# Performance work log

Measured on AMD Instinct MI355X. Metric: run time of the kernel, lower is better.

## Reference

```python
import jax, jax.numpy as jnp
import numpy as np

HEAD_DIM = 64
FEAT_H, FEAT_W = 64, 64
ROPE_THETA = 10000.0


def axial_rope_cache(dim, height, width, theta):
    # Matches compute_axial_rope_cache: interleaved cos/sin of shape [H*W, dim]
    theta_dim = (dim // 2) // 2
    freqs = 1.0 / theta ** (jnp.arange(theta_dim, dtype=jnp.float32) * 2.0 / theta_dim)
    t_x = jnp.tile(jnp.arange(width, dtype=jnp.float32)[None, :], (height, 1)).reshape(-1)
    t_y = jnp.tile(jnp.arange(height, dtype=jnp.float32)[:, None], (1, width)).reshape(-1)
    theta_all = jnp.concatenate([jnp.outer(t_x, freqs), jnp.outer(t_y, freqs)], axis=-1)
    cos = jnp.repeat(jnp.cos(theta_all), 2, axis=-1)  # [H*W, dim]
    sin = jnp.repeat(jnp.sin(theta_all), 2, axis=-1)
    return cos, sin


def apply_rope(x, cos, sin):
    # x: [B, H, N, D]; cos/sin: [N, D]
    x1 = x[..., 0::2]
    x2 = x[..., 1::2]
    rot = jnp.stack([-x2, x1], axis=-1).reshape(x.shape)
    return x * cos[None, None] + rot * sin[None, None]


def setup_inputs() -> dict:
    key = jax.random.key(0)
    ks = jax.random.split(key, 11)
    B, Nq, Nk, E, KVD, ID = 1, 4096, 8192, 256, 64, 256
    s_e = 1.0 / np.sqrt(E)
    s_kv = 1.0 / np.sqrt(KVD)
    s_i = 1.0 / np.sqrt(ID)
    return {
        "query": jax.random.normal(ks[0], (B, Nq, E), jnp.float32),
        "key": jax.random.normal(ks[1], (B, Nk, KVD), jnp.float32),
        "value": jax.random.normal(ks[2], (B, Nk, KVD), jnp.float32),
        "Wq": jax.random.normal(ks[3], (E, ID), jnp.float32) * s_e,
        "bq": jnp.zeros((ID,), jnp.float32),
        "Wk": jax.random.normal(ks[4], (KVD, ID), jnp.float32) * s_kv,
        "bk": jnp.zeros((ID,), jnp.float32),
        "Wv": jax.random.normal(ks[5], (KVD, ID), jnp.float32) * s_kv,
        "bv": jnp.zeros((ID,), jnp.float32),
        "Wo": jax.random.normal(ks[6], (ID, E), jnp.float32) * s_i,
        "bo": jnp.zeros((E,), jnp.float32),
        "num_k_exclude_rope": 0,
    }


def reference(query, key, value, Wq, bq, Wk, bk, Wv, bv, Wo, bo, num_k_exclude_rope):
    B, Nq, _ = query.shape
    Nk = key.shape[1]
    H, D = 4, HEAD_DIM

    def split_heads(x):
        b, n, c = x.shape
        return x.reshape(b, n, H, c // H).transpose(0, 2, 1, 3)

    q = split_heads(query @ Wq + bq)  # [B,H,Nq,D]
    k = split_heads(key @ Wk + bk)    # [B,H,Nk,D]
    v = split_heads(value @ Wv + bv)

    cos, sin = axial_rope_cache(D, FEAT_H, FEAT_W, ROPE_THETA)  # [4096, D]
    q = apply_rope(q, cos, sin)

    num_k_rope = Nk - num_k_exclude_rope
    k_spatial = k[:, :, :num_k_rope, :]
    k_other = k[:, :, num_k_rope:, :]
    repeats = num_k_rope // cos.shape[0]  # rope_k_repeat=True
    cos_k = jnp.tile(cos, (repeats, 1))
    sin_k = jnp.tile(sin, (repeats, 1))
    k_spatial = apply_rope(k_spatial, cos_k, sin_k)
    k = jnp.concatenate([k_spatial, k_other], axis=2)

    q = q / jnp.sqrt(jnp.asarray(D, q.dtype))
    scores = jnp.einsum("bhqd,bhkd->bhqk", q, k)
    attn = jax.nn.softmax(scores, axis=-1)
    out = jnp.einsum("bhqk,bhkd->bhqd", attn, v)
    out = out.transpose(0, 2, 1, 3).reshape(B, Nq, H * D)
    return out @ Wo + bo
```

## Files before the change

kernel.cpp:

```cpp
#include <hip/hip_runtime.h>
#include <hip/hip_bf16.h>

#define NQ 4096
#define NK 8192
#define NSPLIT 8
#define KSPAN (NK / NSPLIT)
#define BK 64

#define QSCALE 0.1803368801111204f

typedef short v8s __attribute__((ext_vector_type(8)));
typedef float v4f __attribute__((ext_vector_type(4)));

static __device__ __forceinline__ unsigned short f2bf(float f) {
    unsigned int u = __float_as_uint(f);
    u = (u + 0x7FFFu + ((u >> 16) & 1u)) >> 16;
    return (unsigned short)u;
}
static __device__ __forceinline__ float bf2f(unsigned short h) {
    return __uint_as_float(((unsigned int)h) << 16);
}
static __device__ __forceinline__ unsigned int pkbf(float a, float b) {
    union { __hip_bfloat162 h; unsigned int u; } cv;
    cv.h = __float22bfloat162_rn(make_float2(a, b));
    return cv.u;
}
static __device__ __forceinline__ void split8(const float* a, v8s& hi, v8s& lo) {
#pragma unroll
    for (int j = 0; j < 8; ++j) {
        unsigned short h = f2bf(a[j]);
        hi[j] = (short)h;
        lo[j] = (short)f2bf(a[j] - bf2f(h));
    }
}
static __device__ __forceinline__ void wgather(const float* __restrict__ W,
                                               int k0, int col, v8s& wh, v8s& wl) {
    float wv[8];
#pragma unroll
    for (int j = 0; j < 8; ++j) wv[j] = W[(size_t)(k0 + j) * 256 + col];
    split8(wv, wh, wl);
}
static __device__ __forceinline__ void dma16(const unsigned short* g, unsigned short* l) {
    __builtin_amdgcn_global_load_lds(
        (const __attribute__((address_space(1))) unsigned int*)(const void*)g,
        (__attribute__((address_space(3))) unsigned int*)(void*)l, 16, 0, 0);
}

__global__ __launch_bounds__(256) void qkv_kernel(
    const float* __restrict__ query, const float* __restrict__ key,
    const float* __restrict__ value,
    const float* __restrict__ Wq, const float* __restrict__ Wk,
    const float* __restrict__ Wv,
    const float* __restrict__ bq, const float* __restrict__ bk,
    const float* __restrict__ bv,
    unsigned short* __restrict__ Qb, unsigned short* __restrict__ Kb,
    unsigned short* __restrict__ Vt, const int* __restrict__ nexp)
{
    const int b = blockIdx.x;
    const int t = threadIdx.x, w = t >> 6, lane = t & 63;
    const int quad = lane >> 4, l16 = lane & 15;
    const int colbase = w * 64;

    if (b < 256) {
        const int n0 = b * 16;
        v4f acc[4];
#pragma unroll
        for (int ct = 0; ct < 4; ++ct) {
            const float bb = bq[colbase + ct * 16 + l16];
            acc[ct] = v4f{bb, bb, bb, bb};
        }
        const float* arow = query + (size_t)(n0 + l16) * 256 + quad * 8;
#pragma unroll
        for (int k0 = 0; k0 < 256; k0 += 32) {
            float av[8];
            *(float4*)av = *(const float4*)(arow + k0);
            *(float4*)(av + 4) = *(const float4*)(arow + k0 + 4);
            v8s ah, al;
            split8(av, ah, al);
#pragma unroll
            for (int ct = 0; ct < 4; ++ct) {
                v8s wh, wl;
                wgather(Wq, k0 + quad * 8, colbase + ct * 16 + l16, wh, wl);
                acc[ct] = __builtin_amdgcn_mfma_f32_16x16x32_bf16(al, wh, acc[ct], 0, 0, 0);
                acc[ct] = __builtin_amdgcn_mfma_f32_16x16x32_bf16(ah, wl, acc[ct], 0, 0, 0);
                acc[ct] = __builtin_amdgcn_mfma_f32_16x16x32_bf16(ah, wh, acc[ct], 0, 0, 0);
            }
        }
#pragma unroll
        for (int ct = 0; ct < 4; ++ct) {
            const int d = ct * 16 + l16;
            const int j = d >> 1;
            const float freq = exp2f(-(float)(j & 15) * 1.66096404744368f);
            const bool isx = (j < 16), odd = (d & 1);
#pragma unroll
            for (int r = 0; r < 4; ++r) {
                const int p = n0 + quad * 4 + r;
                const float tpos = isx ? (float)(p & 63) : (float)(p >> 6);
                float sn, cs;
                __sincosf(tpos * freq, &sn, &cs);
                const float x = acc[ct][r];
                const float xp = __shfl_xor(x, 1, 64);
                const float y = odd ? fmaf(x, cs, xp * sn) : fmaf(x, cs, -xp * sn);
                Qb[((size_t)(w * NQ + p) << 6) + d] = f2bf(y * QSCALE);
            }
        }
    } else {
        const bool isK = (b < 768);
        const int n0 = (isK ? (b - 256) : (b - 768)) * 16;
        const float* X = isK ? key : value;
        const float* W = isK ? Wk : Wv;
        const float* bias = isK ? bk : bv;
        v4f acc[4];
#pragma unroll
        for (int ct = 0; ct < 4; ++ct) {
            const float bb = bias[colbase + ct * 16 + l16];
            acc[ct] = v4f{bb, bb, bb, bb};
        }
        const float* arow = X + (size_t)(n0 + l16) * 64 + quad * 8;
#pragma unroll
        for (int k0 = 0; k0 < 64; k0 += 32) {
            float av[8];
            *(float4*)av = *(const float4*)(arow + k0);
            *(float4*)(av + 4) = *(const float4*)(arow + k0 + 4);
            v8s ah, al;
            split8(av, ah, al);
#pragma unroll
            for (int ct = 0; ct < 4; ++ct) {
                v8s wh, wl;
                wgather(W, k0 + quad * 8, colbase + ct * 16 + l16, wh, wl);
                acc[ct] = __builtin_amdgcn_mfma_f32_16x16x32_bf16(al, wh, acc[ct], 0, 0, 0);
                acc[ct] = __builtin_amdgcn_mfma_f32_16x16x32_bf16(ah, wl, acc[ct], 0, 0, 0);
                acc[ct] = __builtin_amdgcn_mfma_f32_16x16x32_bf16(ah, wh, acc[ct], 0, 0, 0);
            }
        }
        if (isK) {
            const int nro = NK - *nexp;
#pragma unroll
            for (int ct = 0; ct < 4; ++ct) {
                const int d = ct * 16 + l16;
                const int j = d >> 1;
                const float freq = exp2f(-(float)(j & 15) * 1.66096404744368f);
                const bool isx = (j < 16), odd = (d & 1);
#pragma unroll
                for (int r = 0; r < 4; ++r) {
                    const int p = n0 + quad * 4 + r;
                    const int pc = p & 4095;
                    const float tpos = isx ? (float)(pc & 63) : (float)(pc >> 6);
                    float sn, cs;
                    __sincosf(tpos * freq, &sn, &cs);
                    const float x = acc[ct][r];
                    const float xp = __shfl_xor(x, 1, 64);
                    float y = odd ? fmaf(x, cs, xp * sn) : fmaf(x, cs, -xp * sn);
                    y = (p < nro) ? y : x;
                    Kb[((size_t)(w * NK + p) << 6) + d] = f2bf(y);
                }
            }
        } else {
#pragma unroll
            for (int ct = 0; ct < 4; ++ct) {
                const int col = colbase + ct * 16 + l16;
                uint2 u = make_uint2(pkbf(acc[ct][0], acc[ct][1]),
                                     pkbf(acc[ct][2], acc[ct][3]));
                *(uint2*)(Vt + (size_t)col * NK + n0 + quad * 4) = u;
            }
        }
    }
}

__global__ __launch_bounds__(256) void attn_kernel(
    const unsigned short* __restrict__ Qb, const unsigned short* __restrict__ Kb,
    const unsigned short* __restrict__ Vt, unsigned short* __restrict__ Opart,
    float* __restrict__ Lbuf)
{
    __shared__ alignas(16) unsigned short Kl[64 * 64];
    __shared__ alignas(16) unsigned short Vl[64 * 64];

    const int blk = blockIdx.x;
    const int s = blk & 7, h = (blk >> 3) & 3, qt = blk >> 5;
    const int t = threadIdx.x;
    const int w = t >> 6, lane = t & 63;
    const int quad = lane >> 4, l16 = lane & 15;

    const int q0 = qt * 128 + w * 32;
    v8s qf[2][2];
#pragma unroll
    for (int g = 0; g < 2; ++g) {
        const unsigned short* qr = Qb + ((size_t)(h * NQ + q0 + g * 16 + l16) << 6) + quad * 8;
        qf[g][0] = *(const v8s*)qr;
        qf[g][1] = *(const v8s*)(qr + 32);
    }

    v4f O[4][2];
#pragma unroll
    for (int dt = 0; dt < 4; ++dt)
#pragma unroll
        for (int g = 0; g < 2; ++g) O[dt][g] = v4f{0.f, 0.f, 0.f, 0.f};
    float psum[2] = {0.f, 0.f};

    const unsigned short* Kbase = Kb + (((size_t)h * NK + s * KSPAN) << 6);
    const unsigned short* Vbase = Vt + (size_t)(h * 64) * NK + s * KSPAN;

    const int srow = lane >> 3;
    const int schunk = (lane & 7) ^ srow;
    const int c0off = ((quad ^ (l16 & 7)) * 8);
    const int c1off = c0off ^ 32;
    int voff[2][2];
#pragma unroll
    for (int tv = 0; tv < 2; ++tv)
#pragma unroll
        for (int h2 = 0; h2 < 2; ++h2)
            voff[tv][h2] = (((4 * tv + 2 * h2 + (quad >> 1)) ^ (l16 & 7)) << 3) + 4 * (quad & 1);

    for (int k0 = 0; k0 < KSPAN; k0 += BK) {
        __syncthreads();
#pragma unroll
        for (int half = 0; half < 2; ++half) {
            const int r0 = w * 16 + half * 8;
            dma16(Kbase + ((size_t)(k0 + r0 + srow) << 6) + schunk * 8, &Kl[r0 * 64]);
            dma16(Vbase + (size_t)(r0 + srow) * NK + k0 + schunk * 8, &Vl[r0 * 64]);
        }
        __syncthreads();

        v8s pf[2][2];
#pragma unroll
        for (int tt = 0; tt < 4; ++tt) {
            const unsigned short* kr = &Kl[(tt * 16 + l16) * 64];
            const v8s kf0 = *(const v8s*)(kr + c0off);
            const v8s kf1 = *(const v8s*)(kr + c1off);
#pragma unroll
            for (int g = 0; g < 2; ++g) {
                v4f a = v4f{0.f, 0.f, 0.f, 0.f};
                a = __builtin_amdgcn_mfma_f32_16x16x32_bf16(kf0, qf[g][0], a, 0, 0, 0);
                a = __builtin_amdgcn_mfma_f32_16x16x32_bf16(kf1, qf[g][1], a, 0, 0, 0);
                const float e0 = __builtin_amdgcn_exp2f(a[0]);
                const float e1 = __builtin_amdgcn_exp2f(a[1]);
                const float e2 = __builtin_amdgcn_exp2f(a[2]);
                const float e3 = __builtin_amdgcn_exp2f(a[3]);
                psum[g] += (e0 + e1) + (e2 + e3);
                unsigned int* pp = (unsigned int*)&pf[g][tt >> 1];
                pp[(tt & 1) * 2 + 0] = pkbf(e0, e1);
                pp[(tt & 1) * 2 + 1] = pkbf(e2, e3);
            }
        }

#pragma unroll
        for (int dt = 0; dt < 4; ++dt) {
            const unsigned short* vr = &Vl[(dt * 16 + l16) * 64];
#pragma unroll
            for (int tv = 0; tv < 2; ++tv) {
                union { v8s s; uint2 u[2]; } vv;
                vv.u[0] = *(const uint2*)(vr + voff[tv][0]);
                vv.u[1] = *(const uint2*)(vr + voff[tv][1]);
#pragma unroll
                for (int g = 0; g < 2; ++g)
                    O[dt][g] = __builtin_amdgcn_mfma_f32_16x16x32_bf16(vv.s, pf[g][tv], O[dt][g], 0, 0, 0);
            }
        }
    }

#pragma unroll
    for (int g = 0; g < 2; ++g) {
        float p = psum[g];
        p += __shfl_xor(p, 16, 64);
        p += __shfl_xor(p, 32, 64);
        psum[g] = p;
    }
    unsigned short* Ob = Opart + (size_t)blk * 8192;
#pragma unroll
    for (int g = 0; g < 2; ++g) {
        const int row = w * 32 + g * 16 + l16;
#pragma unroll
        for (int dt = 0; dt < 4; ++dt) {
            uint2 u = make_uint2(pkbf(O[dt][g][0], O[dt][g][1]),
                                 pkbf(O[dt][g][2], O[dt][g][3]));
            *(uint2*)(Ob + row * 64 + dt * 16 + quad * 4) = u;
        }
        if (quad == 0) Lbuf[blk * 128 + row] = psum[g];
    }
}

__global__ __launch_bounds__(256) void oproj_kernel(
    const unsigned short* __restrict__ Opart, const float* __restrict__ Lbuf,
    const float* __restrict__ Wo, const float* __restrict__ bo,
    float* __restrict__ out)
{
    const int t = threadIdx.x, w = t >> 6, lane = t & 63;
    const int quad = lane >> 4, l16 = lane & 15;
    const int n0 = blockIdx.x * 16, colbase = w * 64;
    const int qt32 = (n0 >> 7) * 32;
    const int rbase = n0 & 127;

    float linv[4];
#pragma unroll
    for (int hh = 0; hh < 4; ++hh) {
        float ls = 0.f;
#pragma unroll
        for (int sp = 0; sp < NSPLIT; ++sp)
            ls += Lbuf[(qt32 + hh * 8 + sp) * 128 + rbase + l16];
        linv[hh] = 1.f / ls;
    }
    v4f acc[4];
#pragma unroll
    for (int ct = 0; ct < 4; ++ct) {
        const float bb = bo[colbase + ct * 16 + l16];
        acc[ct] = v4f{bb, bb, bb, bb};
    }
#pragma unroll
    for (int k0 = 0; k0 < 256; k0 += 32) {
        const int hh = k0 >> 6;
        const int d0 = (k0 & 63) + quad * 8;
        float av[8] = {0.f, 0.f, 0.f, 0.f, 0.f, 0.f, 0.f, 0.f};
#pragma unroll
        for (int sp = 0; sp < NSPLIT; ++sp) {
            const v8s A = *(const v8s*)(Opart + (size_t)(qt32 + hh * 8 + sp) * 8192
                                        + (rbase + l16) * 64 + d0);
#pragma unroll
            for (int j = 0; j < 8; ++j) av[j] += bf2f((unsigned short)A[j]);
        }
#pragma unroll
        for (int j = 0; j < 8; ++j) av[j] *= linv[hh];
        v8s ah, al;
        split8(av, ah, al);
#pragma unroll
        for (int ct = 0; ct < 4; ++ct) {
            v8s wh, wl;
            wgather(Wo, k0 + quad * 8, colbase + ct * 16 + l16, wh, wl);
            acc[ct] = __builtin_amdgcn_mfma_f32_16x16x32_bf16(al, wh, acc[ct], 0, 0, 0);
            acc[ct] = __builtin_amdgcn_mfma_f32_16x16x32_bf16(ah, wl, acc[ct], 0, 0, 0);
            acc[ct] = __builtin_amdgcn_mfma_f32_16x16x32_bf16(ah, wh, acc[ct], 0, 0, 0);
        }
    }
#pragma unroll
    for (int ct = 0; ct < 4; ++ct)
#pragma unroll
        for (int r = 0; r < 4; ++r)
            out[(size_t)(n0 + quad * 4 + r) * 256 + colbase + ct * 16 + l16] = acc[ct][r];
}

extern "C" void kernel_launch(void* const* d_in, const int* in_sizes, int n_in,
                              void* d_out, int out_size, void* d_ws, size_t ws_size,
                              hipStream_t stream) {
    const float* query = (const float*)d_in[0];
    const float* key   = (const float*)d_in[1];
    const float* value = (const float*)d_in[2];
    const float* Wq    = (const float*)d_in[3];
    const float* bq    = (const float*)d_in[4];
    const float* Wk    = (const float*)d_in[5];
    const float* bk    = (const float*)d_in[6];
    const float* Wv    = (const float*)d_in[7];
    const float* bv    = (const float*)d_in[8];
    const float* Wo    = (const float*)d_in[9];
    const float* bo    = (const float*)d_in[10];
    const int*   nex   = (const int*)d_in[11];

    char* ws = (char*)d_ws;
    unsigned short* Qb    = (unsigned short*)(ws);
    unsigned short* Kb    = (unsigned short*)(ws + (size_t)2 * 1024 * 1024);
    unsigned short* Vt    = (unsigned short*)(ws + (size_t)6 * 1024 * 1024);
    unsigned short* Opart = (unsigned short*)(ws + (size_t)10 * 1024 * 1024);
    float* Lbuf           = (float*)(ws + (size_t)26 * 1024 * 1024);
    float* out            = (float*)d_out;

    qkv_kernel<<<1280, 256, 0, stream>>>(query, key, value, Wq, Wk, Wv,
                                         bq, bk, bv, Qb, Kb, Vt, nex);
    attn_kernel<<<1024, 256, 0, stream>>>(Qb, Kb, Vt, Opart, Lbuf);
    oproj_kernel<<<256, 256, 0, stream>>>(Opart, Lbuf, Wo, bo, out);
}
```

Before: 168.4 us.

## Pre-split weights into bf16 hi/lo fragment layout and split O reduction from projection

Adds a prep kernel that converts every weight matrix once per call into packed bf16 hi/lo fragments laid out for the MFMA operand, so the GEMM kernels do one vector load instead of eight strided scalar loads plus a split. The partial-output reduction and normalisation move into a separate oreduce kernel that writes hi/lo activations. oproj is reshaped to 1024 smaller blocks that each compute one column tile, giving more parallelism. This adds two kernel launches and an extra round trip through global memory for the reduced output.

After: 158.9 us. 1.06x faster.

```diff
diff --git a/kernel.cpp b/kernel.cpp
--- a/kernel.cpp
+++ b/kernel.cpp
@@ -33,12 +33,12 @@
         lo[j] = (short)f2bf(a[j] - bf2f(h));
     }
 }
-static __device__ __forceinline__ void wgather(const float* __restrict__ W,
-                                               int k0, int col, v8s& wh, v8s& wl) {
-    float wv[8];
-#pragma unroll
-    for (int j = 0; j < 8; ++j) wv[j] = W[(size_t)(k0 + j) * 256 + col];
-    split8(wv, wh, wl);
+static __device__ __forceinline__ void wload(const unsigned short* __restrict__ H,
+                                             const unsigned short* __restrict__ L,
+                                             int k0, int col, v8s& wh, v8s& wl) {
+    const size_t f = (size_t)((k0 >> 3) * 256 + col) * 8;
+    wh = *(const v8s*)(H + f);
+    wl = *(const v8s*)(L + f);
 }
 static __device__ __forceinline__ void dma16(const unsigned short* g, unsigned short* l) {
     __builtin_amdgcn_global_load_lds(
@@ -46,11 +46,38 @@
         (__attribute__((address_space(3))) unsigned int*)(void*)l, 16, 0, 0);
 }
 
+__global__ __launch_bounds__(256) void prep_kernel(
+    const float* __restrict__ Wq, const float* __restrict__ Wk,
+    const float* __restrict__ Wv, const float* __restrict__ Wo,
+    unsigned short* __restrict__ WqH, unsigned short* __restrict__ WqL,
+    unsigned short* __restrict__ WkH, unsigned short* __restrict__ WkL,
+    unsigned short* __restrict__ WvH, unsigned short* __restrict__ WvL,
+    unsigned short* __restrict__ WoH, unsigned short* __restrict__ WoL)
+{
+    const int tid = blockIdx.x * 256 + threadIdx.x;
+    const float* W;
+    unsigned short *H, *L;
+    int f;
+    if (tid < 8192)        { W = Wq; H = WqH; L = WqL; f = tid; }
+    else if (tid < 10240)  { W = Wk; H = WkH; L = WkL; f = tid - 8192; }
+    else if (tid < 12288)  { W = Wv; H = WvH; L = WvL; f = tid - 10240; }
+    else                   { W = Wo; H = WoH; L = WoL; f = tid - 12288; }
+    const int col = f & 255, k0 = (f >> 8) << 3;
+    float wv[8];
+#pragma unroll
+    for (int j = 0; j < 8; ++j) wv[j] = W[(size_t)(k0 + j) * 256 + col];
+    v8s hi, lo;
+    split8(wv, hi, lo);
+    *(v8s*)(H + (size_t)f * 8) = hi;
+    *(v8s*)(L + (size_t)f * 8) = lo;
+}
+
 __global__ __launch_bounds__(256) void qkv_kernel(
     const float* __restrict__ query, const float* __restrict__ key,
     const float* __restrict__ value,
-    const float* __restrict__ Wq, const float* __restrict__ Wk,
-    const float* __restrict__ Wv,
+    const unsigned short* __restrict__ WqH, const unsigned short* __restrict__ WqL,
+    const unsigned short* __restrict__ WkH, const unsigned short* __restrict__ WkL,
+    const unsigned short* __restrict__ WvH, const unsigned short* __restrict__ WvL,
     const float* __restrict__ bq, const float* __restrict__ bk,
     const float* __restrict__ bv,
     unsigned short* __restrict__ Qb, unsigned short* __restrict__ Kb,
@@ -80,7 +107,7 @@
 #pragma unroll
             for (int ct = 0; ct < 4; ++ct) {
                 v8s wh, wl;
-                wgather(Wq, k0 + quad * 8, colbase + ct * 16 + l16, wh, wl);
+                wload(WqH, WqL, k0 + quad * 8, colbase + ct * 16 + l16, wh, wl);
                 acc[ct] = __builtin_amdgcn_mfma_f32_16x16x32_bf16(al, wh, acc[ct], 0, 0, 0);
                 acc[ct] = __builtin_amdgcn_mfma_f32_16x16x32_bf16(ah, wl, acc[ct], 0, 0, 0);
                 acc[ct] = __builtin_amdgcn_mfma_f32_16x16x32_bf16(ah, wh, acc[ct], 0, 0, 0);
@@ -108,7 +135,8 @@
         const bool isK = (b < 768);
         const int n0 = (isK ? (b - 256) : (b - 768)) * 16;
         const float* X = isK ? key : value;
-        const float* W = isK ? Wk : Wv;
+        const unsigned short* WH = isK ? WkH : WvH;
+        const unsigned short* WL = isK ? WkL : WvL;
         const float* bias = isK ? bk : bv;
         v4f acc[4];
 #pragma unroll
@@ -127,7 +155,7 @@
 #pragma unroll
             for (int ct = 0; ct < 4; ++ct) {
                 v8s wh, wl;
-                wgather(W, k0 + quad * 8, colbase + ct * 16 + l16, wh, wl);
+                wload(WH, WL, k0 + quad * 8, colbase + ct * 16 + l16, wh, wl);
                 acc[ct] = __builtin_amdgcn_mfma_f32_16x16x32_bf16(al, wh, acc[ct], 0, 0, 0);
                 acc[ct] = __builtin_amdgcn_mfma_f32_16x16x32_bf16(ah, wl, acc[ct], 0, 0, 0);
                 acc[ct] = __builtin_amdgcn_mfma_f32_16x16x32_bf16(ah, wh, acc[ct], 0, 0, 0);
@@ -279,62 +307,61 @@
     }
 }
 
+__global__ __launch_bounds__(256) void oreduce_kernel(
+    const unsigned short* __restrict__ Opart, const float* __restrict__ Lbuf,
+    unsigned short* __restrict__ OredH, unsigned short* __restrict__ OredL)
+{
+    const int tid = blockIdx.x * 256 + threadIdx.x;
+    const int e0 = tid << 3;
+    const int r = e0 >> 8, d0 = e0 & 255;
+    const int h = d0 >> 6;
+    const int qt = r >> 7, rr = r & 127;
+    const int base = qt * 32 + h * 8;
+    const unsigned short* op = Opart + (size_t)base * 8192 + rr * 64 + (d0 & 63);
+    float lsum = 0.f;
+    float o[8] = {0.f, 0.f, 0.f, 0.f, 0.f, 0.f, 0.f, 0.f};
+#pragma unroll
+    for (int s = 0; s < NSPLIT; ++s) {
+        lsum += Lbuf[(base + s) * 128 + rr];
+        v8s a = *(const v8s*)(op + (size_t)s * 8192);
+#pragma unroll
+        for (int j = 0; j < 8; ++j) o[j] += bf2f((unsigned short)a[j]);
+    }
+    const float inv = 1.f / lsum;
+#pragma unroll
+    for (int j = 0; j < 8; ++j) o[j] *= inv;
+    v8s hi, lo;
+    split8(o, hi, lo);
+    *(v8s*)(OredH + (size_t)r * 256 + d0) = hi;
+    *(v8s*)(OredL + (size_t)r * 256 + d0) = lo;
+}
+
 __global__ __launch_bounds__(256) void oproj_kernel(
-    const unsigned short* __restrict__ Opart, const float* __restrict__ Lbuf,
-    const float* __restrict__ Wo, const float* __restrict__ bo,
-    float* __restrict__ out)
+    const unsigned short* __restrict__ OredH, const unsigned short* __restrict__ OredL,
+    const unsigned short* __restrict__ WoH, const unsigned short* __restrict__ WoL,
+    const float* __restrict__ bo, float* __restrict__ out)
 {
     const int t = threadIdx.x, w = t >> 6, lane = t & 63;
     const int quad = lane >> 4, l16 = lane & 15;
-    const int n0 = blockIdx.x * 16, colbase = w * 64;
-    const int qt32 = (n0 >> 7) * 32;
-    const int rbase = n0 & 127;
-
-    float linv[4];
-#pragma unroll
-    for (int hh = 0; hh < 4; ++hh) {
-        float ls = 0.f;
-#pragma unroll
-        for (int sp = 0; sp < NSPLIT; ++sp)
-            ls += Lbuf[(qt32 + hh * 8 + sp) * 128 + rbase + l16];
-        linv[hh] = 1.f / ls;
-    }
-    v4f acc[4];
-#pragma unroll
-    for (int ct = 0; ct < 4; ++ct) {
-        const float bb = bo[colbase + ct * 16 + l16];
-        acc[ct] = v4f{bb, bb, bb, bb};
-    }
+    const int n0 = (blockIdx.x >> 2) * 16;
+    const int col = (blockIdx.x & 3) * 64 + w * 16 + l16;
+    const float bb = bo[col];
+    v4f acc = v4f{bb, bb, bb, bb};
+    const unsigned short* ah_row = OredH + (size_t)(n0 + l16) * 256 + quad * 8;
+    const unsigned short* al_row = OredL + (size_t)(n0 + l16) * 256 + quad * 8;
 #pragma unroll
     for (int k0 = 0; k0 < 256; k0 += 32) {
-        const int hh = k0 >> 6;
-        const int d0 = (k0 & 63) + quad * 8;
-        float av[8] = {0.f, 0.f, 0.f, 0.f, 0.f, 0.f, 0.f, 0.f};
-#pragma unroll
-        for (int sp = 0; sp < NSPLIT; ++sp) {
-            const v8s A = *(const v8s*)(Opart + (size_t)(qt32 + hh * 8 + sp) * 8192
-                                        + (rbase + l16) * 64 + d0);
-#pragma unroll
-            for (int j = 0; j < 8; ++j) av[j] += bf2f((unsigned short)A[j]);
-        }
-#pragma unroll
-        for (int j = 0; j < 8; ++j) av[j] *= linv[hh];
-        v8s ah, al;
-        split8(av, ah, al);
-#pragma unroll
-        for (int ct = 0; ct < 4; ++ct) {
-            v8s wh, wl;
-            wgather(Wo, k0 + quad * 8, colbase + ct * 16 + l16, wh, wl);
-            acc[ct] = __builtin_amdgcn_mfma_f32_16x16x32_bf16(al, wh, acc[ct], 0, 0, 0);
-            acc[ct] = __builtin_amdgcn_mfma_f32_16x16x32_bf16(ah, wl, acc[ct], 0, 0, 0);
-            acc[ct] = __builtin_amdgcn_mfma_f32_16x16x32_bf16(ah, wh, acc[ct], 0, 0, 0);
-        }
-    }
-#pragma unroll
-    for (int ct = 0; ct < 4; ++ct)
-#pragma unroll
-        for (int r = 0; r < 4; ++r)
-            out[(size_t)(n0 + quad * 4 + r) * 256 + colbase + ct * 16 + l16] = acc[ct][r];
+        v8s ah = *(const v8s*)(ah_row + k0);
+        v8s al = *(const v8s*)(al_row + k0);
+        v8s wh, wl;
+        wload(WoH, WoL, k0 + quad * 8, col, wh, wl);
+        acc = __builtin_amdgcn_mfma_f32_16x16x32_bf16(al, wh, acc, 0, 0, 0);
+        acc = __builtin_amdgcn_mfma_f32_16x16x32_bf16(ah, wl, acc, 0, 0, 0);
+        acc = __builtin_amdgcn_mfma_f32_16x16x32_bf16(ah, wh, acc, 0, 0, 0);
+    }
+#pragma unroll
+    for (int r = 0; r < 4; ++r)
+        out[(size_t)(n0 + quad * 4 + r) * 256 + col] = acc[r];
 }
 
 extern "C" void kernel_launch(void* const* d_in, const int* in_sizes, int n_in,
@@ -354,15 +381,31 @@
     const int*   nex   = (const int*)d_in[11];
 
     char* ws = (char*)d_ws;
+    const size_t MB = 1024 * 1024;
     unsigned short* Qb    = (unsigned short*)(ws);
-    unsigned short* Kb    = (unsigned short*)(ws + (size_t)2 * 1024 * 1024);
-    unsigned short* Vt    = (unsigned short*)(ws + (size_t)6 * 1024 * 1024);
-    unsigned short* Opart = (unsigned short*)(ws + (size_t)10 * 1024 * 1024);
-    float* Lbuf           = (float*)(ws + (size_t)26 * 1024 * 1024);
-    float* out            = (float*)d_out;
-
-    qkv_kernel<<<1280, 256, 0, stream>>>(query, key, value, Wq, Wk, Wv,
+    unsigned short* Kb    = (unsigned short*)(ws + 2 * MB);
+    unsigned short* Vt    = (unsigned short*)(ws + 6 * MB);
+    unsigned short* Opart = (unsigned short*)(ws + 10 * MB);
+    float* Lbuf           = (float*)(ws + 26 * MB);
+    unsigned short* OredH = (unsigned short*)(ws + 26 * MB + 512 * 1024);
+    unsigned short* OredL = (unsigned short*)(ws + 28 * MB + 512 * 1024);
+    unsigned short* Wpl   = (unsigned short*)(ws + 30 * MB + 512 * 1024);
+    unsigned short* WqH = Wpl;
+    unsigned short* WqL = Wpl + 65536;
+    unsigned short* WkH = Wpl + 131072;
+    unsigned short* WkL = Wpl + 147456;
+    unsigned short* WvH = Wpl + 163840;
+    unsigned short* WvL = Wpl + 180224;
+    unsigned short* WoH = Wpl + 196608;
+    unsigned short* WoL = Wpl + 262144;
+    float* out = (float*)d_out;
+
+    prep_kernel<<<80, 256, 0, stream>>>(Wq, Wk, Wv, Wo,
+                                        WqH, WqL, WkH, WkL, WvH, WvL, WoH, WoL);
+    qkv_kernel<<<1280, 256, 0, stream>>>(query, key, value,
+                                         WqH, WqL, WkH, WkL, WvH, WvL,
                                          bq, bk, bv, Qb, Kb, Vt, nex);
     attn_kernel<<<1024, 256, 0, stream>>>(Qb, Kb, Vt, Opart, Lbuf);
-    oproj_kernel<<<256, 256, 0, stream>>>(Opart, Lbuf, Wo, bo, out);
-}
+    oreduce_kernel<<<512, 256, 0, stream>>>(Opart, Lbuf, OredH, OredL);
+    oproj_kernel<<<1024, 256, 0, stream>>>(OredH, OredL, WoH, WoL, bo, out);
+}
```
